# Optimization experiments

Measured on AMD Instinct MI355X. Metric: run time of the kernel, lower is better.

The kernel has to match this reference:

```python
import jax, jax.numpy as jnp
import numpy as np

N_NODES = 50000
N_EDGES = 600000
D = 128          # in = hidden = out (forced by residual adds)
HEADS = 4
HEAD_DIM = D // HEADS
EPS = 1e-5
NEG_SLOPE = 0.2  # PyG GATConv default


def setup_inputs() -> dict:
    key = jax.random.key(0)
    ks = jax.random.split(key, 12)
    s = 1.0 / np.sqrt(D)
    x = jax.random.normal(ks[0], (N_NODES, D), dtype=jnp.float32)
    edge_index = jax.random.randint(ks[1], (2, N_EDGES), 0, N_NODES, dtype=jnp.int32)
    # conv1: GATConv(D, D//heads, heads=heads)
    W1 = jax.random.normal(ks[2], (D, D), dtype=jnp.float32) * s
    a_src1 = jax.random.normal(ks[3], (HEADS, HEAD_DIM), dtype=jnp.float32) * s
    a_dst1 = jax.random.normal(ks[4], (HEADS, HEAD_DIM), dtype=jnp.float32) * s
    b1 = jnp.zeros((D,), dtype=jnp.float32)
    # conv2: GATConv(D, D, heads=1)
    W2 = jax.random.normal(ks[5], (D, D), dtype=jnp.float32) * s
    a_src2 = jax.random.normal(ks[6], (1, D), dtype=jnp.float32) * s
    a_dst2 = jax.random.normal(ks[7], (1, D), dtype=jnp.float32) * s
    b2 = jnp.zeros((D,), dtype=jnp.float32)
    # shared AddAndNorm BatchNorm1d params (same module used twice)
    bn_gamma = jnp.ones((D,), dtype=jnp.float32)
    bn_beta = jnp.zeros((D,), dtype=jnp.float32)
    return {"x": x, "edge_index": edge_index,
            "W1": W1, "a_src1": a_src1, "a_dst1": a_dst1, "b1": b1,
            "W2": W2, "a_src2": a_src2, "a_dst2": a_dst2, "b2": b2,
            "bn_gamma": bn_gamma, "bn_beta": bn_beta}


def _gat_conv(x, W, a_src, a_dst, b, src, dst, heads, head_dim):
    n = x.shape[0]
    h = (x @ W).reshape(n, heads, head_dim)                 # [N,H,C]
    e_src = jnp.einsum('nhc,hc->nh', h, a_src)              # [N,H]
    e_dst = jnp.einsum('nhc,hc->nh', h, a_dst)
    e = jax.nn.leaky_relu(e_src[src] + e_dst[dst], NEG_SLOPE)  # [E,H]
    # segment softmax over incoming edges per destination node
    m = jax.ops.segment_max(e, dst, num_segments=n)
    alpha = jnp.exp(e - m[dst])
    denom = jax.ops.segment_sum(alpha, dst, num_segments=n)
    alpha = alpha / denom[dst]
    out = jax.ops.segment_sum(alpha[:, :, None] * h[src], dst, num_segments=n)
    return out.reshape(n, heads * head_dim) + b


def _batch_norm(x, gamma, beta):
    mean = jnp.mean(x, axis=0)
    var = jnp.var(x, axis=0)
    return (x - mean) * jax.lax.rsqrt(var + EPS) * gamma + beta


def reference(x, edge_index, W1, a_src1, a_dst1, b1, W2, a_src2, a_dst2, b2,
              bn_gamma, bn_beta):
    n = x.shape[0]
    # PyG GATConv adds self loops by default
    loops = jnp.arange(n, dtype=edge_index.dtype)
    src = jnp.concatenate([edge_index[0], loops])
    dst = jnp.concatenate([edge_index[1], loops])

    res = x
    h = _gat_conv(x, W1, a_src1, a_dst1, b1, src, dst, HEADS, HEAD_DIM)
    h = _batch_norm(h + res, bn_gamma, bn_beta)   # dropout is identity (eval)
    h = jax.nn.relu(h)
    res = h
    h = _gat_conv(h, W2, a_src2, a_dst2, b2, src, dst, 1, D)
    h = _batch_norm(h + res, bn_gamma, bn_beta)
    return h
```

## Files before the change

kernel.cpp:

```cpp
#include <hip/hip_runtime.h>
#include <math.h>

#define NN 50000
#define NE 600000
#define ET (NE + NN)
#define D 128
#define EPSB 1e-5f
#define SLOPE 0.2f
#define XPITCH 136
#define SCB 196

typedef float f32x4 __attribute__((ext_vector_type(4)));
typedef short bf16x8 __attribute__((ext_vector_type(8)));

__device__ inline unsigned short bf16r(float f) {
    unsigned int u = __float_as_uint(f);
    unsigned int r = (u + 0x7fff + ((u >> 16) & 1)) >> 16;
    return (unsigned short)r;
}
__device__ inline float bflo(unsigned int u) { return __uint_as_float(u << 16); }
__device__ inline float bfhi(unsigned int u) { return __uint_as_float(u & 0xffff0000u); }
__device__ inline float lrelu(float e) { return (e > 0.f) ? e : SLOPE * e; }

__global__ void hist_kernel(const int* __restrict__ ei, int* __restrict__ deg) {
    int e = blockIdx.x * blockDim.x + threadIdx.x;
    if (e >= ET) return;
    int dst = (e < NE) ? ei[NE + e] : (e - NE);
    atomicAdd(&deg[dst], 1);
}

__global__ __launch_bounds__(256) void scan_a_kernel(const int* __restrict__ deg,
                                                     int* __restrict__ tmp,
                                                     int* __restrict__ bsum) {
    __shared__ int sm[256];
    int t = threadIdx.x;
    int idx = blockIdx.x * 256 + t;
    int v = (idx < NN) ? deg[idx] : 0;
    sm[t] = v;
    __syncthreads();
    #pragma unroll
    for (int d = 1; d < 256; d <<= 1) {
        int add = (t >= d) ? sm[t - d] : 0;
        __syncthreads();
        sm[t] += add;
        __syncthreads();
    }
    if (idx < NN) tmp[idx] = sm[t];
    if (t == 255) bsum[blockIdx.x] = sm[255];
}

__global__ __launch_bounds__(256) void scan_b_kernel(const int* __restrict__ deg,
                                                     const int* __restrict__ tmp,
                                                     const int* __restrict__ bsum,
                                                     int* __restrict__ offs,
                                                     int* __restrict__ cur) {
    __shared__ int sm[256];
    int t = threadIdx.x;
    sm[t] = (t < SCB) ? bsum[t] : 0;
    __syncthreads();
    #pragma unroll
    for (int d = 1; d < 256; d <<= 1) {
        int add = (t >= d) ? sm[t - d] : 0;
        __syncthreads();
        sm[t] += add;
        __syncthreads();
    }
    int bpre = (blockIdx.x == 0) ? 0 : sm[blockIdx.x - 1];
    int idx = blockIdx.x * 256 + t;
    if (idx < NN) {
        int excl = bpre + tmp[idx] - deg[idx];
        offs[idx] = excl;
        cur[idx] = excl;
        if (idx == NN - 1) offs[NN] = bpre + tmp[idx];
    }
}

__global__ void scatter_kernel(const int* __restrict__ ei, int* __restrict__ cur,
                               unsigned short* __restrict__ ssrc) {
    int e = blockIdx.x * blockDim.x + threadIdx.x;
    if (e >= ET) return;
    int src, dst;
    if (e < NE) { src = ei[e]; dst = ei[NE + e]; }
    else        { src = dst = e - NE; }
    int pos = atomicAdd(&cur[dst], 1);
    ssrc[pos] = (unsigned short)src;
}

__global__ void wconv_kernel(const float* __restrict__ W1, const float* __restrict__ W2,
                             unsigned short* __restrict__ wt1, unsigned short* __restrict__ wt2) {
    int t = blockIdx.x * blockDim.x + threadIdx.x;
    if (t >= 2 * D * D) return;
    int i = (t < D * D) ? t : t - D * D;
    int n = i >> 7, k = i & 127;
    if (t < D * D) wt1[i] = bf16r(W1[k * D + n]);
    else           wt2[i] = bf16r(W2[k * D + n]);
}

template <bool BNRELU>
__global__ __launch_bounds__(256) void gemm_mfma_kernel(const float* __restrict__ X,
                                                        const unsigned short* __restrict__ Wt,
                                                        const float* __restrict__ scsh,
                                                        unsigned short* __restrict__ Hb, int nrows) {
    __shared__ unsigned short Xl[64 * XPITCH];
    __shared__ unsigned short Wl[128 * XPITCH];
    int t = threadIdx.x;
    int row0 = blockIdx.x * 64;

    {
        int r = t >> 1, cb = (t & 1) * 64;
        const uint4* src = (const uint4*)&Wt[r * D + cb];
        uint4* dst = (uint4*)&Wl[r * XPITCH + cb];
        #pragma unroll
        for (int j = 0; j < 8; ++j) dst[j] = src[j];
    }
    {
        int r = t >> 2, cb = (t & 3) * 32;
        int gr = row0 + r; if (gr >= nrows) gr = nrows - 1;
        const float4* src = (const float4*)&X[(long)gr * D + cb];
        #pragma unroll
        for (int j = 0; j < 8; ++j) {
            float4 v = src[j];
            if (BNRELU) {
                float4 g = *(const float4*)&scsh[cb + j * 4];
                float4 s = *(const float4*)&scsh[D + cb + j * 4];
                v.x = fmaxf(fmaf(v.x, g.x, s.x), 0.f);
                v.y = fmaxf(fmaf(v.y, g.y, s.y), 0.f);
                v.z = fmaxf(fmaf(v.z, g.z, s.z), 0.f);
                v.w = fmaxf(fmaf(v.w, g.w, s.w), 0.f);
            }
            ushort4 p;
            p.x = bf16r(v.x); p.y = bf16r(v.y);
            p.z = bf16r(v.z); p.w = bf16r(v.w);
            *(ushort4*)&Xl[r * XPITCH + cb + j * 4] = p;
        }
    }
    __syncthreads();

    int wv = t >> 6, l = t & 63;
    int lr = l & 15, lg = l >> 4;
    f32x4 acc[8];
    #pragma unroll
    for (int n = 0; n < 8; ++n) acc[n] = (f32x4){0.f, 0.f, 0.f, 0.f};

    #pragma unroll
    for (int kc = 0; kc < 4; ++kc) {
        bf16x8 a = *(const bf16x8*)&Xl[(wv * 16 + lr) * XPITCH + kc * 32 + lg * 8];
        #pragma unroll
        for (int n = 0; n < 8; ++n) {
            bf16x8 b = *(const bf16x8*)&Wl[(n * 16 + lr) * XPITCH + kc * 32 + lg * 8];
            acc[n] = __builtin_amdgcn_mfma_f32_16x16x32_bf16(a, b, acc[n], 0, 0, 0);
        }
    }
    int growb = row0 + wv * 16 + lg * 4;
    #pragma unroll
    for (int n = 0; n < 8; ++n) {
        #pragma unroll
        for (int j = 0; j < 4; ++j) {
            int gr = growb + j;
            if (gr < nrows) Hb[(long)gr * D + n * 16 + lr] = bf16r(acc[n][j]);
        }
    }
}

template <int H>
__global__ void logits_kernel(const unsigned short* __restrict__ Hb,
                              const float* __restrict__ a_src,
                              const float* __restrict__ a_dst,
                              float* __restrict__ es, float* __restrict__ ed) {
    int i = blockIdx.x * blockDim.x + threadIdx.x;
    if (i >= NN * H) return;
    int n = i / H, h = i % H;
    const int CH = D / H;
    const unsigned short* hp = Hb + (long)n * D + h * CH;
    const float* as = a_src + h * CH;
    const float* ad = a_dst + h * CH;
    float s = 0.f, d = 0.f;
    for (int c = 0; c < CH; c += 8) {
        uint4 u = *(const uint4*)&hp[c];
        float4 a0 = *(const float4*)&as[c];
        float4 a1 = *(const float4*)&as[c + 4];
        float4 b0 = *(const float4*)&ad[c];
        float4 b1 = *(const float4*)&ad[c + 4];
        float f0 = bflo(u.x), f1 = bfhi(u.x), f2 = bflo(u.y), f3 = bfhi(u.y);
        float f4 = bflo(u.z), f5 = bfhi(u.z), f6 = bflo(u.w), f7 = bfhi(u.w);
        s += f0 * a0.x + f1 * a0.y + f2 * a0.z + f3 * a0.w
           + f4 * a1.x + f5 * a1.y + f6 * a1.z + f7 * a1.w;
        d += f0 * b0.x + f1 * b0.y + f2 * b0.z + f3 * b0.w
           + f4 * b1.x + f5 * b1.y + f6 * b1.z + f7 * b1.w;
    }
    es[i] = s; ed[i] = d;
}

template <int H, bool RECON>
__global__ __launch_bounds__(256) void agg_kernel(const unsigned short* __restrict__ Hb,
                                                  const float* __restrict__ es,
                                                  const float* __restrict__ ed,
                                                  const int* __restrict__ offs,
                                                  const unsigned short* __restrict__ ssrc,
                                                  const float* __restrict__ bias,
                                                  const float* __restrict__ resid,
                                                  const float* __restrict__ scsh,
                                                  float* __restrict__ out) {
    const int CHK = 64 / H;
    int wave = threadIdx.x >> 6;
    int lane = threadIdx.x & 63;
    int dst = blockIdx.x * 4 + wave;
    if (dst >= NN) return;
    int h  = (H == 1) ? 0 : (lane >> 4);
    int hh = lane & (H - 1);
    int fo = lane * 2;
    int beg = offs[dst], end = offs[dst + 1];
    int cnt = end - beg;
    float edv = ed[dst * H + hh];

    float ax0 = 0.f, ay0 = 0.f, ax1 = 0.f, ay1 = 0.f;
    float ds0 = 0.f, ds1 = 0.f;

    for (int base = 0; base < cnt; base += CHK) {
        int j = lane / H;
        float w = 0.f;
        int msrc = 0;
        if (base + j < cnt) {
            msrc = ssrc[beg + base + j];
            w = __expf(lrelu(es[msrc * H + hh] + edv));
        }
        int lim = min(CHK, cnt - base);
        int jj = 0;
        for (; jj + 1 < lim; jj += 2) {
            float w0 = __shfl(w, jj * H + h);
            float w1 = __shfl(w, (jj + 1) * H + h);
            int s0 = __shfl(msrc, jj * H);
            int s1 = __shfl(msrc, (jj + 1) * H);
            unsigned int u0 = *(const unsigned int*)&Hb[(long)s0 * D + fo];
            unsigned int u1 = *(const unsigned int*)&Hb[(long)s1 * D + fo];
            ax0 += w0 * bflo(u0); ay0 += w0 * bfhi(u0); ds0 += w0;
            ax1 += w1 * bflo(u1); ay1 += w1 * bfhi(u1); ds1 += w1;
        }
        if (jj < lim) {
            float w0 = __shfl(w, jj * H + h);
            int s0 = __shfl(msrc, jj * H);
            unsigned int u0 = *(const unsigned int*)&Hb[(long)s0 * D + fo];
            ax0 += w0 * bflo(u0); ay0 += w0 * bfhi(u0); ds0 += w0;
        }
    }
    float dsum = ds0 + ds1;
    float accx = ax0 + ax1;
    float accy = ay0 + ay1;
    float inv = 1.0f / dsum;
    float2 rr = *(const float2*)&resid[(long)dst * D + fo];
    if (RECON) {
        float2 g = *(const float2*)&scsh[fo];
        float2 s = *(const float2*)&scsh[D + fo];
        rr.x = fmaxf(fmaf(rr.x, g.x, s.x), 0.f);
        rr.y = fmaxf(fmaf(rr.y, g.y, s.y), 0.f);
    }
    float2 o;
    o.x = accx * inv + bias[fo]     + rr.x;
    o.y = accy * inv + bias[fo + 1] + rr.y;
    *(float2*)&out[(long)dst * D + fo] = o;
}

__global__ __launch_bounds__(128) void stats_kernel(const float* __restrict__ y,
                                                    float* __restrict__ st) {
    int f = threadIdx.x;
    float s = 0.f, q = 0.f;
    for (int r = blockIdx.x; r < NN; r += gridDim.x) {
        float v = y[(long)r * D + f];
        s += v; q += v * v;
    }
    atomicAdd(&st[f], s);
    atomicAdd(&st[D + f], q);
}

__global__ void finalize_kernel(const float* __restrict__ st,
                                const float* __restrict__ gamma,
                                const float* __restrict__ beta,
                                float* __restrict__ scsh) {
    int f = threadIdx.x;
    if (f >= D) return;
    float mean = st[f] * (1.0f / NN);
    float var = st[D + f] * (1.0f / NN) - mean * mean;
    float g = gamma[f] * rsqrtf(var + EPSB);
    scsh[f] = g;
    scsh[D + f] = beta[f] - mean * g;
}

template <bool RELU>
__global__ __launch_bounds__(256) void apply_kernel(const float* __restrict__ y,
                                                    const float* __restrict__ st,
                                                    const float* __restrict__ gamma,
                                                    const float* __restrict__ beta,
                                                    float* __restrict__ out) {
    long i = (long)(blockIdx.x * blockDim.x + threadIdx.x) * 4;
    if (i >= (long)NN * D) return;
    int f = (int)(i & (D - 1));
    const float invn = 1.0f / NN;
    float4 sv = *(const float4*)&st[f];
    float4 qv = *(const float4*)&st[D + f];
    float4 gv = *(const float4*)&gamma[f];
    float4 bv = *(const float4*)&beta[f];
    float4 v = *(const float4*)&y[i];
    float4 o;
    float m, vr, g;
    m = sv.x * invn; vr = qv.x * invn - m * m; g = gv.x * rsqrtf(vr + EPSB);
    o.x = (v.x - m) * g + bv.x;
    m = sv.y * invn; vr = qv.y * invn - m * m; g = gv.y * rsqrtf(vr + EPSB);
    o.y = (v.y - m) * g + bv.y;
    m = sv.z * invn; vr = qv.z * invn - m * m; g = gv.z * rsqrtf(vr + EPSB);
    o.z = (v.z - m) * g + bv.z;
    m = sv.w * invn; vr = qv.w * invn - m * m; g = gv.w * rsqrtf(vr + EPSB);
    o.w = (v.w - m) * g + bv.w;
    if (RELU) {
        o.x = fmaxf(o.x, 0.f); o.y = fmaxf(o.y, 0.f);
        o.z = fmaxf(o.z, 0.f); o.w = fmaxf(o.w, 0.f);
    }
    *(float4*)&out[i] = o;
}

extern "C" void kernel_launch(void* const* d_in, const int* in_sizes, int n_in,
                              void* d_out, int out_size, void* d_ws, size_t ws_size,
                              hipStream_t stream) {
    const float* x      = (const float*)d_in[0];
    const int*   ei     = (const int*)  d_in[1];
    const float* W1     = (const float*)d_in[2];
    const float* a_src1 = (const float*)d_in[3];
    const float* a_dst1 = (const float*)d_in[4];
    const float* b1     = (const float*)d_in[5];
    const float* W2     = (const float*)d_in[6];
    const float* a_src2 = (const float*)d_in[7];
    const float* a_dst2 = (const float*)d_in[8];
    const float* b2     = (const float*)d_in[9];
    const float* gamma  = (const float*)d_in[10];
    const float* beta   = (const float*)d_in[11];
    float* out = (float*)d_out;

    unsigned short* Hb = (unsigned short*)d_ws;
    float* B    = (float*)d_ws + 3200000;
    float* es1  = B + 6400000;
    float* ed1  = es1 + 200000;
    float* es2  = ed1 + 200000;
    float* ed2  = es2 + 50000;
    float* st1  = ed2 + 50000;
    float* st2  = st1 + 256;
    float* scsh1= st2 + 256;
    int*   deg  = (int*)(scsh1 + 256);
    int*   offs = deg + NN;
    int*   cur  = offs + NN + 1;
    int*   tmp  = cur + NN;
    int*   bsum = tmp + NN;
    unsigned short* ssrc = (unsigned short*)(bsum + SCB + 4);
    unsigned short* wt1  = ssrc + ((ET + 7) & ~7);
    unsigned short* wt2  = wt1 + D * D;

    hipMemsetAsync(deg, 0, NN * sizeof(int), stream);
    hipMemsetAsync(st1, 0, 512 * sizeof(float), stream);

    wconv_kernel<<<(2 * D * D + 255) / 256, 256, 0, stream>>>(W1, W2, wt1, wt2);
    hist_kernel<<<(ET + 255) / 256, 256, 0, stream>>>(ei, deg);
    scan_a_kernel<<<SCB, 256, 0, stream>>>(deg, tmp, bsum);
    scan_b_kernel<<<SCB, 256, 0, stream>>>(deg, tmp, bsum, offs, cur);
    scatter_kernel<<<(ET + 255) / 256, 256, 0, stream>>>(ei, cur, ssrc);

    const int GG = (NN + 63) / 64;
    gemm_mfma_kernel<false><<<GG, 256, 0, stream>>>(x, wt1, nullptr, Hb, NN);
    logits_kernel<4><<<(NN * 4 + 255) / 256, 256, 0, stream>>>(Hb, a_src1, a_dst1, es1, ed1);
    agg_kernel<4, false><<<(NN + 3) / 4, 256, 0, stream>>>(Hb, es1, ed1, offs, ssrc, b1, x, nullptr, B);
    stats_kernel<<<1024, 128, 0, stream>>>(B, st1);
    finalize_kernel<<<1, 128, 0, stream>>>(st1, gamma, beta, scsh1);

    gemm_mfma_kernel<true><<<GG, 256, 0, stream>>>(B, wt2, scsh1, Hb, NN);
    logits_kernel<1><<<(NN + 255) / 256, 256, 0, stream>>>(Hb, a_src2, a_dst2, es2, ed2);
    agg_kernel<1, true><<<(NN + 3) / 4, 256, 0, stream>>>(Hb, es2, ed2, offs, ssrc, b2, B, scsh1, out);
    stats_kernel<<<1024, 128, 0, stream>>>(out, st2);
    apply_kernel<false><<<(NN * D / 4 + 255) / 256, 256, 0, stream>>>(out, st2, gamma, beta, out);
}
```

Measured before the change: 369.8 us.

## Fuse logits into GEMM epilogue, store layer-1 output as bf16, merge setup kernels

New measurement: 357.0 us. 1.04x faster.

```diff
diff --git a/kernel.cpp b/kernel.cpp
--- a/kernel.cpp
+++ b/kernel.cpp
@@ -20,7 +20,27 @@
 }
 __device__ inline float bflo(unsigned int u) { return __uint_as_float(u << 16); }
 __device__ inline float bfhi(unsigned int u) { return __uint_as_float(u & 0xffff0000u); }
+__device__ inline float b2f(unsigned short u) { return __uint_as_float(((unsigned int)u) << 16); }
 __device__ inline float lrelu(float e) { return (e > 0.f) ? e : SLOPE * e; }
+
+__global__ __launch_bounds__(256) void setup_kernel(const float* __restrict__ W1,
+                                                    const float* __restrict__ W2,
+                                                    unsigned short* __restrict__ wt1,
+                                                    unsigned short* __restrict__ wt2,
+                                                    int* __restrict__ deg,
+                                                    float* __restrict__ stz) {
+    int t = blockIdx.x * blockDim.x + threadIdx.x;
+    if (t < NN) deg[t] = 0;
+    if (t < 512) stz[t] = 0.f;
+    if (t < D * D) {
+        int n = t >> 7, k = t & 127;
+        wt1[t] = bf16r(W1[k * D + n]);
+    } else if (t < 2 * D * D) {
+        int i = t - D * D;
+        int n = i >> 7, k = i & 127;
+        wt2[i] = bf16r(W2[k * D + n]);
+    }
+}
 
 __global__ void hist_kernel(const int* __restrict__ ei, int* __restrict__ deg) {
     int e = blockIdx.x * blockDim.x + threadIdx.x;
@@ -86,26 +106,28 @@
     ssrc[pos] = (unsigned short)src;
 }
 
-__global__ void wconv_kernel(const float* __restrict__ W1, const float* __restrict__ W2,
-                             unsigned short* __restrict__ wt1, unsigned short* __restrict__ wt2) {
-    int t = blockIdx.x * blockDim.x + threadIdx.x;
-    if (t >= 2 * D * D) return;
-    int i = (t < D * D) ? t : t - D * D;
-    int n = i >> 7, k = i & 127;
-    if (t < D * D) wt1[i] = bf16r(W1[k * D + n]);
-    else           wt2[i] = bf16r(W2[k * D + n]);
-}
-
-template <bool BNRELU>
-__global__ __launch_bounds__(256) void gemm_mfma_kernel(const float* __restrict__ X,
-                                                        const unsigned short* __restrict__ Wt,
-                                                        const float* __restrict__ scsh,
-                                                        unsigned short* __restrict__ Hb, int nrows) {
+template <int H, bool BNRELU>
+__global__ __launch_bounds__(256) void gemm_mfma_kernel(
+        const float* __restrict__ Xf, const unsigned short* __restrict__ Xb,
+        const unsigned short* __restrict__ Wt,
+        const float* __restrict__ st, const float* __restrict__ gamma,
+        const float* __restrict__ beta,
+        const float* __restrict__ a_src, const float* __restrict__ a_dst,
+        unsigned short* __restrict__ Hb, float* __restrict__ es, float* __restrict__ ed,
+        int nrows) {
     __shared__ unsigned short Xl[64 * XPITCH];
     __shared__ unsigned short Wl[128 * XPITCH];
+    __shared__ float scshl[256];
     int t = threadIdx.x;
     int row0 = blockIdx.x * 64;
 
+    if (BNRELU && t < 128) {
+        float mean = st[t] * (1.0f / NN);
+        float var = st[128 + t] * (1.0f / NN) - mean * mean;
+        float g = gamma[t] * rsqrtf(var + EPSB);
+        scshl[t] = g;
+        scshl[128 + t] = beta[t] - mean * g;
+    }
     {
         int r = t >> 1, cb = (t & 1) * 64;
         const uint4* src = (const uint4*)&Wt[r * D + cb];
@@ -113,25 +135,38 @@
         #pragma unroll
         for (int j = 0; j < 8; ++j) dst[j] = src[j];
     }
+    if (BNRELU) __syncthreads();
     {
         int r = t >> 2, cb = (t & 3) * 32;
         int gr = row0 + r; if (gr >= nrows) gr = nrows - 1;
-        const float4* src = (const float4*)&X[(long)gr * D + cb];
-        #pragma unroll
-        for (int j = 0; j < 8; ++j) {
-            float4 v = src[j];
-            if (BNRELU) {
-                float4 g = *(const float4*)&scsh[cb + j * 4];
-                float4 s = *(const float4*)&scsh[D + cb + j * 4];
-                v.x = fmaxf(fmaf(v.x, g.x, s.x), 0.f);
-                v.y = fmaxf(fmaf(v.y, g.y, s.y), 0.f);
-                v.z = fmaxf(fmaf(v.z, g.z, s.z), 0.f);
-                v.w = fmaxf(fmaf(v.w, g.w, s.w), 0.f);
+        if (!BNRELU) {
+            const float4* src = (const float4*)&Xf[(long)gr * D + cb];
+            #pragma unroll
+            for (int j = 0; j < 8; ++j) {
+                float4 v = src[j];
+                ushort4 p;
+                p.x = bf16r(v.x); p.y = bf16r(v.y);
+                p.z = bf16r(v.z); p.w = bf16r(v.w);
+                *(ushort4*)&Xl[r * XPITCH + cb + j * 4] = p;
             }
-            ushort4 p;
-            p.x = bf16r(v.x); p.y = bf16r(v.y);
-            p.z = bf16r(v.z); p.w = bf16r(v.w);
-            *(ushort4*)&Xl[r * XPITCH + cb + j * 4] = p;
+        } else {
+            #pragma unroll
+            for (int j = 0; j < 4; ++j) {
+                uint4 u = *(const uint4*)&Xb[(long)gr * D + cb + j * 8];
+                unsigned int uu0 = u.x, uu1 = u.y, uu2 = u.z, uu3 = u.w;
+                ushort4 p0, p1;
+                int fb = cb + j * 8;
+                p0.x = bf16r(fmaxf(fmaf(bflo(uu0), scshl[fb+0], scshl[128+fb+0]), 0.f));
+                p0.y = bf16r(fmaxf(fmaf(bfhi(uu0), scshl[fb+1], scshl[128+fb+1]), 0.f));
+                p0.z = bf16r(fmaxf(fmaf(bflo(uu1), scshl[fb+2], scshl[128+fb+2]), 0.f));
+                p0.w = bf16r(fmaxf(fmaf(bfhi(uu1), scshl[fb+3], scshl[128+fb+3]), 0.f));
+                p1.x = bf16r(fmaxf(fmaf(bflo(uu2), scshl[fb+4], scshl[128+fb+4]), 0.f));
+                p1.y = bf16r(fmaxf(fmaf(bfhi(uu2), scshl[fb+5], scshl[128+fb+5]), 0.f));
+                p1.z = bf16r(fmaxf(fmaf(bflo(uu3), scshl[fb+6], scshl[128+fb+6]), 0.f));
+                p1.w = bf16r(fmaxf(fmaf(bfhi(uu3), scshl[fb+7], scshl[128+fb+7]), 0.f));
+                *(ushort4*)&Xl[r * XPITCH + fb] = p0;
+                *(ushort4*)&Xl[r * XPITCH + fb + 4] = p1;
+            }
         }
     }
     __syncthreads();
@@ -151,56 +186,62 @@
             acc[n] = __builtin_amdgcn_mfma_f32_16x16x32_bf16(a, b, acc[n], 0, 0, 0);
         }
     }
-    int growb = row0 + wv * 16 + lg * 4;
+    __syncthreads();
+    int trow0 = wv * 16 + lg * 4;
+    int growb = row0 + trow0;
     #pragma unroll
     for (int n = 0; n < 8; ++n) {
         #pragma unroll
         for (int j = 0; j < 4; ++j) {
+            unsigned short us = bf16r(acc[n][j]);
+            Xl[(trow0 + j) * XPITCH + n * 16 + lr] = us;
             int gr = growb + j;
-            if (gr < nrows) Hb[(long)gr * D + n * 16 + lr] = bf16r(acc[n][j]);
-        }
-    }
-}
-
-template <int H>
-__global__ void logits_kernel(const unsigned short* __restrict__ Hb,
-                              const float* __restrict__ a_src,
-                              const float* __restrict__ a_dst,
-                              float* __restrict__ es, float* __restrict__ ed) {
-    int i = blockIdx.x * blockDim.x + threadIdx.x;
-    if (i >= NN * H) return;
-    int n = i / H, h = i % H;
-    const int CH = D / H;
-    const unsigned short* hp = Hb + (long)n * D + h * CH;
-    const float* as = a_src + h * CH;
-    const float* ad = a_dst + h * CH;
-    float s = 0.f, d = 0.f;
-    for (int c = 0; c < CH; c += 8) {
-        uint4 u = *(const uint4*)&hp[c];
-        float4 a0 = *(const float4*)&as[c];
-        float4 a1 = *(const float4*)&as[c + 4];
-        float4 b0 = *(const float4*)&ad[c];
-        float4 b1 = *(const float4*)&ad[c + 4];
-        float f0 = bflo(u.x), f1 = bfhi(u.x), f2 = bflo(u.y), f3 = bfhi(u.y);
-        float f4 = bflo(u.z), f5 = bfhi(u.z), f6 = bflo(u.w), f7 = bfhi(u.w);
-        s += f0 * a0.x + f1 * a0.y + f2 * a0.z + f3 * a0.w
-           + f4 * a1.x + f5 * a1.y + f6 * a1.z + f7 * a1.w;
-        d += f0 * b0.x + f1 * b0.y + f2 * b0.z + f3 * b0.w
-           + f4 * b1.x + f5 * b1.y + f6 * b1.z + f7 * b1.w;
-    }
-    es[i] = s; ed[i] = d;
-}
-
-template <int H, bool RECON>
-__global__ __launch_bounds__(256) void agg_kernel(const unsigned short* __restrict__ Hb,
-                                                  const float* __restrict__ es,
-                                                  const float* __restrict__ ed,
-                                                  const int* __restrict__ offs,
-                                                  const unsigned short* __restrict__ ssrc,
-                                                  const float* __restrict__ bias,
-                                                  const float* __restrict__ resid,
-                                                  const float* __restrict__ scsh,
-                                                  float* __restrict__ out) {
+            if (gr < nrows) Hb[(long)gr * D + n * 16 + lr] = us;
+        }
+    }
+    __syncthreads();
+    {
+        int rl = l >> 2, q = l & 3;
+        int trow = wv * 16 + rl;
+        int gr = row0 + trow;
+        const unsigned short* cp = &Xl[trow * XPITCH + q * 32];
+        const float* as = a_src + q * 32;
+        const float* ad = a_dst + q * 32;
+        float s = 0.f, d2 = 0.f;
+        #pragma unroll
+        for (int c = 0; c < 32; c += 8) {
+            uint4 u = *(const uint4*)&cp[c];
+            float4 a0 = *(const float4*)&as[c];
+            float4 a1 = *(const float4*)&as[c + 4];
+            float4 b0 = *(const float4*)&ad[c];
+            float4 b1 = *(const float4*)&ad[c + 4];
+            float f0 = bflo(u.x), f1 = bfhi(u.x), f2 = bflo(u.y), f3 = bfhi(u.y);
+            float f4 = bflo(u.z), f5 = bfhi(u.z), f6 = bflo(u.w), f7 = bfhi(u.w);
+            s  += f0*a0.x + f1*a0.y + f2*a0.z + f3*a0.w
+                + f4*a1.x + f5*a1.y + f6*a1.z + f7*a1.w;
+            d2 += f0*b0.x + f1*b0.y + f2*b0.z + f3*b0.w
+                + f4*b1.x + f5*b1.y + f6*b1.z + f7*b1.w;
+        }
+        if (H == 4) {
+            if (gr < nrows) { es[gr * 4 + q] = s; ed[gr * 4 + q] = d2; }
+        } else {
+            s  += __shfl_xor(s, 1);  s  += __shfl_xor(s, 2);
+            d2 += __shfl_xor(d2, 1); d2 += __shfl_xor(d2, 2);
+            if (q == 0 && gr < nrows) { es[gr] = s; ed[gr] = d2; }
+        }
+    }
+}
+
+template <int H, bool RECON, bool OUTBF16>
+__global__ __launch_bounds__(256) void agg_kernel(
+        const unsigned short* __restrict__ Hb,
+        const float* __restrict__ es, const float* __restrict__ ed,
+        const int* __restrict__ offs, const unsigned short* __restrict__ ssrc,
+        const float* __restrict__ bias,
+        const float* __restrict__ residf, const unsigned short* __restrict__ residb,
+        const float* __restrict__ st, const float* __restrict__ gamma,
+        const float* __restrict__ beta,
+        float* __restrict__ outf, unsigned short* __restrict__ outb) {
     const int CHK = 64 / H;
     int wave = threadIdx.x >> 6;
     int lane = threadIdx.x & 63;
@@ -247,45 +288,49 @@
     float accx = ax0 + ax1;
     float accy = ay0 + ay1;
     float inv = 1.0f / dsum;
-    float2 rr = *(const float2*)&resid[(long)dst * D + fo];
+    float rx, ry;
     if (RECON) {
-        float2 g = *(const float2*)&scsh[fo];
-        float2 s = *(const float2*)&scsh[D + fo];
-        rr.x = fmaxf(fmaf(rr.x, g.x, s.x), 0.f);
-        rr.y = fmaxf(fmaf(rr.y, g.y, s.y), 0.f);
-    }
-    float2 o;
-    o.x = accx * inv + bias[fo]     + rr.x;
-    o.y = accy * inv + bias[fo + 1] + rr.y;
-    *(float2*)&out[(long)dst * D + fo] = o;
-}
-
-__global__ __launch_bounds__(128) void stats_kernel(const float* __restrict__ y,
+        unsigned int ur = *(const unsigned int*)&residb[(long)dst * D + fo];
+        float y0 = bflo(ur), y1 = bfhi(ur);
+        float m0 = st[fo] * (1.0f / NN);
+        float v0 = st[128 + fo] * (1.0f / NN) - m0 * m0;
+        float g0 = gamma[fo] * rsqrtf(v0 + EPSB);
+        float s0v = beta[fo] - m0 * g0;
+        float m1 = st[fo + 1] * (1.0f / NN);
+        float v1 = st[128 + fo + 1] * (1.0f / NN) - m1 * m1;
+        float g1 = gamma[fo + 1] * rsqrtf(v1 + EPSB);
+        float s1v = beta[fo + 1] - m1 * g1;
+        rx = fmaxf(fmaf(y0, g0, s0v), 0.f);
+        ry = fmaxf(fmaf(y1, g1, s1v), 0.f);
+    } else {
+        float2 r2 = *(const float2*)&residf[(long)dst * D + fo];
+        rx = r2.x; ry = r2.y;
+    }
+    float ox = accx * inv + bias[fo]     + rx;
+    float oy = accy * inv + bias[fo + 1] + ry;
+    if (OUTBF16) {
+        unsigned int pk = (unsigned int)bf16r(ox) | ((unsigned int)bf16r(oy) << 16);
+        *(unsigned int*)&outb[(long)dst * D + fo] = pk;
+    } else {
+        float2 o; o.x = ox; o.y = oy;
+        *(float2*)&outf[(long)dst * D + fo] = o;
+    }
+}
+
+template <bool BF16IN>
+__global__ __launch_bounds__(128) void stats_kernel(const float* __restrict__ yf,
+                                                    const unsigned short* __restrict__ yb,
                                                     float* __restrict__ st) {
     int f = threadIdx.x;
     float s = 0.f, q = 0.f;
     for (int r = blockIdx.x; r < NN; r += gridDim.x) {
-        float v = y[(long)r * D + f];
+        float v = BF16IN ? b2f(yb[(long)r * D + f]) : yf[(long)r * D + f];
         s += v; q += v * v;
     }
     atomicAdd(&st[f], s);
     atomicAdd(&st[D + f], q);
 }
 
-__global__ void finalize_kernel(const float* __restrict__ st,
-                                const float* __restrict__ gamma,
-                                const float* __restrict__ beta,
-                                float* __restrict__ scsh) {
-    int f = threadIdx.x;
-    if (f >= D) return;
-    float mean = st[f] * (1.0f / NN);
-    float var = st[D + f] * (1.0f / NN) - mean * mean;
-    float g = gamma[f] * rsqrtf(var + EPSB);
-    scsh[f] = g;
-    scsh[D + f] = beta[f] - mean * g;
-}
-
-template <bool RELU>
 __global__ __launch_bounds__(256) void apply_kernel(const float* __restrict__ y,
                                                     const float* __restrict__ st,
                                                     const float* __restrict__ gamma,
@@ -310,10 +355,6 @@
     o.z = (v.z - m) * g + bv.z;
     m = sv.w * invn; vr = qv.w * invn - m * m; g = gv.w * rsqrtf(vr + EPSB);
     o.w = (v.w - m) * g + bv.w;
-    if (RELU) {
-        o.x = fmaxf(o.x, 0.f); o.y = fmaxf(o.y, 0.f);
-        o.z = fmaxf(o.z, 0.f); o.w = fmaxf(o.w, 0.f);
-    }
     *(float4*)&out[i] = o;
 }
 
@@ -335,42 +376,39 @@
     float* out = (float*)d_out;
 
     unsigned short* Hb = (unsigned short*)d_ws;
-    float* B    = (float*)d_ws + 3200000;
-    float* es1  = B + 6400000;
+    unsigned short* Bb = Hb + 6400000;
+    float* es1  = (float*)(Bb + 6400000);
     float* ed1  = es1 + 200000;
     float* es2  = ed1 + 200000;
     float* ed2  = es2 + 50000;
     float* st1  = ed2 + 50000;
     float* st2  = st1 + 256;
-    float* scsh1= st2 + 256;
-    int*   deg  = (int*)(scsh1 + 256);
+    unsigned short* wt1 = (unsigned short*)(st2 + 256);
+    unsigned short* wt2 = wt1 + D * D;
+    int*   deg  = (int*)(wt2 + D * D);
     int*   offs = deg + NN;
     int*   cur  = offs + NN + 1;
     int*   tmp  = cur + NN;
     int*   bsum = tmp + NN;
     unsigned short* ssrc = (unsigned short*)(bsum + SCB + 4);
-    unsigned short* wt1  = ssrc + ((ET + 7) & ~7);
-    unsigned short* wt2  = wt1 + D * D;
-
-    hipMemsetAsync(deg, 0, NN * sizeof(int), stream);
-    hipMemsetAsync(st1, 0, 512 * sizeof(float), stream);
-
-    wconv_kernel<<<(2 * D * D + 255) / 256, 256, 0, stream>>>(W1, W2, wt1, wt2);
+
+    setup_kernel<<<SCB, 256, 0, stream>>>(W1, W2, wt1, wt2, deg, st1);
     hist_kernel<<<(ET + 255) / 256, 256, 0, stream>>>(ei, deg);
     scan_a_kernel<<<SCB, 256, 0, stream>>>(deg, tmp, bsum);
     scan_b_kernel<<<SCB, 256, 0, stream>>>(deg, tmp, bsum, offs, cur);
     scatter_kernel<<<(ET + 255) / 256, 256, 0, stream>>>(ei, cur, ssrc);
 
     const int GG = (NN + 63) / 64;
-    gemm_mfma_kernel<false><<<GG, 256, 0, stream>>>(x, wt1, nullptr, Hb, NN);
-    logits_kernel<4><<<(NN * 4 + 255) / 256, 256, 0, stream>>>(Hb, a_src1, a_dst1, es1, ed1);
-    agg_kernel<4, false><<<(NN + 3) / 4, 256, 0, stream>>>(Hb, es1, ed1, offs, ssrc, b1, x, nullptr, B);
-    stats_kernel<<<1024, 128, 0, stream>>>(B, st1);
-    finalize_kernel<<<1, 128, 0, stream>>>(st1, gamma, beta, scsh1);
-
-    gemm_mfma_kernel<true><<<GG, 256, 0, stream>>>(B, wt2, scsh1, Hb, NN);
-    logits_kernel<1><<<(NN + 255) / 256, 256, 0, stream>>>(Hb, a_src2, a_dst2, es2, ed2);
-    agg_kernel<1, true><<<(NN + 3) / 4, 256, 0, stream>>>(Hb, es2, ed2, offs, ssrc, b2, B, scsh1, out);
-    stats_kernel<<<1024, 128, 0, stream>>>(out, st2);
-    apply_kernel<false><<<(NN * D / 4 + 255) / 256, 256, 0, stream>>>(out, st2, gamma, beta, out);
-}
+    gemm_mfma_kernel<4, false><<<GG, 256, 0, stream>>>(
+        x, nullptr, wt1, nullptr, nullptr, nullptr, a_src1, a_dst1, Hb, es1, ed1, NN);
+    agg_kernel<4, false, true><<<(NN + 3) / 4, 256, 0, stream>>>(
+        Hb, es1, ed1, offs, ssrc, b1, x, nullptr, nullptr, nullptr, nullptr, nullptr, Bb);
+    stats_kernel<true><<<1024, 128, 0, stream>>>(nullptr, Bb, st1);
+
+    gemm_mfma_kernel<1, true><<<GG, 256, 0, stream>>>(
+        nullptr, Bb, wt2, st1, gamma, beta, a_src2, a_dst2, Hb, es2, ed2, NN);
+    agg_kernel<1, true, false><<<(NN + 3) / 4, 256, 0, stream>>>(
+        Hb, es2, ed2, offs, ssrc, b2, nullptr, Bb, st1, gamma, beta, out, nullptr);
+    stats_kernel<false><<<1024, 128, 0, stream>>>(out, nullptr, st2);
+    apply_kernel<<<(NN * D / 4 + 255) / 256, 256, 0, stream>>>(out, st2, gamma, beta, out);
+}
```
